# Kernel tuning notes

Hardware: AMD Instinct MI355X
Metric: run time of the kernel (lower is better)

Reference implementation:

```python
import jax, jax.numpy as jnp
import numpy as np

EPS2D = 0.3          # gsplat classic-mode 2D blur added to covariance diagonal
SZ2 = 0.001 ** 2     # sigma_z^2 from the fixed z-scale 0.001
ALPHA_MAX = 0.999    # gsplat alpha clamp


def setup_inputs() -> dict:
    key = jax.random.key(0)
    k0, k1, k2, k3, k4 = jax.random.split(key, 5)
    B, N, H, W = 2, 768, 160, 160
    means = jax.random.uniform(k0, (B, N, 2), jnp.float32, 0.0, float(W))      # pixel coords
    scales = jax.random.uniform(k1, (B, N, 2), jnp.float32, 1.0, 8.0)          # pixel scales
    rotations = jax.random.normal(k2, (B, N, 1), jnp.float32)                  # radians
    colors = jax.random.uniform(k3, (B, N, 3), jnp.float32)                    # RGB [0,1]
    opacities = jax.random.uniform(k4, (B, N, 1), jnp.float32)                 # [0,1]
    return {"means": means, "scales": scales, "rotations": rotations,
            "colors": colors, "opacities": opacities, "H": H, "W": W}


def reference(means, scales, rotations, colors, opacities, H, W):
    B, N, _ = means.shape
    dt = means.dtype
    # quat (cos t/2, 0, 0, sin t/2) == rotation about z by t; cov3d = R diag(sx^2,sy^2,sz^2) R^T
    theta = rotations[..., 0]
    c, s = jnp.cos(theta), jnp.sin(theta)
    sx2, sy2 = scales[..., 0] ** 2, scales[..., 1] ** 2
    a = c * c * sx2 + s * s * sy2            # xy-block of 3D covariance
    b = c * s * (sx2 - sy2)
    d = s * s * sx2 + c * c * sy2
    mx, my = means[..., 0], means[..., 1]
    # viewmat=I, K=I, z=1 -> projected mean = (x, y); Jacobian J = [[1,0,-x],[0,1,-y]]
    # cov2d = J cov3d J^T + eps2d * I  (z-block contributes sz^2 * [x,y] outer [x,y])
    cov_xx = a + SZ2 * mx * mx + EPS2D
    cov_xy = b + SZ2 * mx * my
    cov_yy = d + SZ2 * my * my + EPS2D
    det = cov_xx * cov_yy - cov_xy * cov_xy
    ca, cb, cc = cov_yy / det, -cov_xy / det, cov_xx / det   # conic (inverse cov)

    px = jnp.arange(W, dtype=dt) + 0.5       # pixel centers
    py = jnp.arange(H, dtype=dt) + 0.5
    gx, gy = jnp.meshgrid(px, py)            # (H, W)
    dx = gx.reshape(-1)[None, :, None] - mx[:, None, :]      # (B, HW, N)
    dy = gy.reshape(-1)[None, :, None] - my[:, None, :]
    q = (ca[:, None, :] * dx * dx
         + 2.0 * cb[:, None, :] * dx * dy
         + cc[:, None, :] * dy * dy)
    alpha = jnp.minimum(opacities[:, None, :, 0] * jnp.exp(-0.5 * q), ALPHA_MAX)

    # front-to-back compositing (all depths == 1 -> stable input order)
    log1m = jnp.log1p(-alpha)                                 # (B, HW, N)
    T = jnp.exp(jnp.cumsum(log1m, axis=-1) - log1m)           # exclusive cumprod of (1-alpha)
    w = alpha * T                                             # per-gaussian pixel weight
    img = jnp.einsum('bpn,bnc->bpc', w, colors)               # (B, HW, 3)
    img = img.reshape(B, H, W, 3).transpose(0, 3, 1, 2)       # (B, 3, H, W)
    return jnp.clip(img, 0.0, 1.0)
```

## Files before the change

kernel.cpp:

```cpp
#include <hip/hip_runtime.h>
#include <hip/hip_fp16.h>
#include <string.h>

#define BATCH   2
#define NG      768
#define H_      160
#define W_      160
#define NPIX    (H_ * W_)
#define NCHUNK  8
#define CHUNK   (NG / NCHUNK)
#define TILE    8
#define TPD     (W_ / TILE)
#define NTILE   (TPD * TPD)
#define EPS2D_  0.3f
#define SZ2_    1.0e-6f
#define ALPHA_MAX_ 0.999f
#define KEXP    (-0.7213475204444817f)
#define LN_CULL_EPS (-13.815511f)


__global__ __launch_bounds__(256)
void gr_precompute(const float* __restrict__ means,
                   const float* __restrict__ scales,
                   const float* __restrict__ rots,
                   const float* __restrict__ colors,
                   const float* __restrict__ opac,
                   float4* __restrict__ cull, float4* __restrict__ pay, int total) {
    int i = blockIdx.x * blockDim.x + threadIdx.x;
    if (i >= total) return;
    float theta = rots[i];
    float c = cosf(theta), s = sinf(theta);
    float sx = scales[2*i], sy = scales[2*i+1];
    float sx2 = sx*sx, sy2 = sy*sy;
    float a  = c*c*sx2 + s*s*sy2;
    float bb = c*s*(sx2 - sy2);
    float d  = s*s*sx2 + c*c*sy2;
    float mx = means[2*i], my = means[2*i+1];
    float cxx = a + SZ2_*mx*mx + EPS2D_;
    float cxy = bb + SZ2_*mx*my;
    float cyy = d + SZ2_*my*my + EPS2D_;
    float det = cxx*cyy - cxy*cxy;
    float inv = 1.0f / det;
    float ca  =  cyy * inv;
    float cb2 = -cxy * inv;
    float cc  =  cxx * inv;
    float op  = opac[i];

    float k2 = 2.0f * (logf(op) - LN_CULL_EPS);
    k2 = fmaxf(k2, 0.0f);
    float kk = sqrtf(k2);
    float ex = kk * sqrtf(cxx);
    float ey = kk * sqrtf(cyy);
    cull[i] = make_float4(mx, my, ex, ey);

    float A = KEXP * ca;
    float B = KEXP * 2.0f * cb2;
    float C = KEXP * cc;
    float D = KEXP * (-2.0f * ca * mx - 2.0f * cb2 * my);
    float E = KEXP * (-2.0f * cc * my - 2.0f * cb2 * mx);
    float F = KEXP * (ca*mx*mx + 2.0f*cb2*mx*my + cc*my*my) + log2f(op);
    float cr = colors[3*i], cg = colors[3*i+1], cb = colors[3*i+2];
    __half2 h2 = __floats2half2_rn(cr, cg);
    float rg; memcpy(&rg, &h2, 4);
    pay[2*i]   = make_float4(A, B, C, D);
    pay[2*i+1] = make_float4(E, F, rg, cb);
}

__global__ __launch_bounds__(256)
void gr_render(const float4* __restrict__ cull, const float4* __restrict__ pay,
               float* __restrict__ out) {
    __shared__ float4 stage[4][CHUNK * 2];
    __shared__ float4 partl[4][64];
    int tid  = threadIdx.x;
    int wave = tid >> 6;
    int lane = tid & 63;
    int tile = blockIdx.x;
    int b    = blockIdx.y;
    int tx = tile % TPD, ty = tile / TPD;
    int pxi = tx * TILE + (lane & 7);
    int pyi = ty * TILE + (lane >> 3);
    float px = (float)pxi + 0.5f;
    float py = (float)pyi + 0.5f;
    float cxm = (float)(tx * TILE) + 0.5f * TILE;
    float cym = (float)(ty * TILE) + 0.5f * TILE;
    const float RH = 0.5f * TILE;
    float x2 = px*px, xy = px*py, y2 = py*py;

    float R = 0.f, G = 0.f, B = 0.f, T = 1.f;

    #pragma unroll
    for (int cc = 0; cc < 2; ++cc) {
        int chunk = wave * 2 + cc;
        int base  = b * NG + chunk * CHUNK;
        int cnt = 0;

        {
            float4 cu = cull[base + lane];
            bool keep = (fabsf(cu.x - cxm) <= cu.z + RH) &&
                        (fabsf(cu.y - cym) <= cu.w + RH);
            unsigned long long m = __ballot(keep);
            unsigned pre = __builtin_amdgcn_mbcnt_hi((unsigned)(m >> 32),
                            __builtin_amdgcn_mbcnt_lo((unsigned)m, 0u));
            if (keep) {
                int gi = base + lane;
                stage[wave][2*pre]     = pay[2*gi];
                stage[wave][2*pre + 1] = pay[2*gi + 1];
            }
            cnt = (int)__popcll(m);
        }
        {
            bool valid = lane < (CHUNK - 64);
            int gi = base + 64 + (valid ? lane : 0);
            float4 cu = cull[gi];
            bool keep = valid &&
                        (fabsf(cu.x - cxm) <= cu.z + RH) &&
                        (fabsf(cu.y - cym) <= cu.w + RH);
            unsigned long long m = __ballot(keep);
            unsigned pre = __builtin_amdgcn_mbcnt_hi((unsigned)(m >> 32),
                            __builtin_amdgcn_mbcnt_lo((unsigned)m, 0u));
            if (keep) {
                int slot = cnt + (int)pre;
                stage[wave][2*slot]     = pay[2*gi];
                stage[wave][2*slot + 1] = pay[2*gi + 1];
            }
            cnt += (int)__popcll(m);
        }

        for (int i = 0; i < cnt; ++i) {
            float4 av = stage[wave][2*i];
            float4 ev = stage[wave][2*i + 1];
            float q = fmaf(av.x, x2,
                      fmaf(av.y, xy,
                      fmaf(av.z, y2,
                      fmaf(av.w, px,
                      fmaf(ev.x, py, ev.y)))));
            float al = fminf(__builtin_exp2f(q), ALPHA_MAX_);
            float w  = T * al;
            __half2 h2; memcpy(&h2, &ev.z, 4);
            float2 rg = __half22float2(h2);
            R  = fmaf(w, rg.x, R);
            G  = fmaf(w, rg.y, G);
            B  = fmaf(w, ev.w, B);
            T -= w;
            if (((i & 7) == 7) && __all(T < 1.0e-4f)) break;
        }
        if (__all(T < 1.0e-4f)) break;
    }

    partl[wave][lane] = make_float4(R, G, B, T);
    __syncthreads();

    float4 o = partl[3][lane];
    float r = o.x, g = o.y, bb = o.z;
    #pragma unroll
    for (int i = 2; i >= 0; --i) {
        float4 oi = partl[i][lane];
        r  = fmaf(oi.w, r,  oi.x);
        g  = fmaf(oi.w, g,  oi.y);
        bb = fmaf(oi.w, bb, oi.z);
    }
    if (wave < 3) {
        float v = (wave == 0) ? r : (wave == 1) ? g : bb;
        v = fminf(fmaxf(v, 0.f), 1.f);
        out[(b * 3 + wave) * NPIX + pyi * W_ + pxi] = v;
    }
}

extern "C" void kernel_launch(void* const* d_in, const int* in_sizes, int n_in,
                              void* d_out, int out_size, void* d_ws, size_t ws_size,
                              hipStream_t stream) {
    const float* means  = (const float*)d_in[0];
    const float* scales = (const float*)d_in[1];
    const float* rots   = (const float*)d_in[2];
    const float* colors = (const float*)d_in[3];
    const float* opac   = (const float*)d_in[4];
    float* out = (float*)d_out;

    int total = BATCH * NG;
    float4* cullA = (float4*)d_ws;
    float4* pay   = cullA + total;

    gr_precompute<<<(total + 255) / 256, 256, 0, stream>>>(
        means, scales, rots, colors, opac, cullA, pay, total);

    dim3 rgrid(NTILE, BATCH);
    gr_render<<<rgrid, 256, 0, stream>>>(cullA, pay, out);
}
```

Before: 73.65 us.

## Fuse per-gaussian precompute into render kernel with 8 waves per tile

```diff
diff --git a/kernel.cpp b/kernel.cpp
--- a/kernel.cpp
+++ b/kernel.cpp
@@ -7,8 +7,8 @@
 #define H_      160
 #define W_      160
 #define NPIX    (H_ * W_)
-#define NCHUNK  8
-#define CHUNK   (NG / NCHUNK)
+#define NWAVE   8
+#define CHUNK   (NG / NWAVE)
 #define TILE    8
 #define TPD     (W_ / TILE)
 #define NTILE   (TPD * TPD)
@@ -18,64 +18,61 @@
 #define KEXP    (-0.7213475204444817f)
 #define LN_CULL_EPS (-13.815511f)
 
+__global__ __launch_bounds__(512)
+void gr_fused(const float* __restrict__ means,
+              const float* __restrict__ scales,
+              const float* __restrict__ rots,
+              const float* __restrict__ colors,
+              const float* __restrict__ opac,
+              float* __restrict__ out) {
+    __shared__ float4 ldsCull[NG];
+    __shared__ float4 ldsPay[NG * 2];
+    __shared__ int    ldsIdx[NWAVE][CHUNK];
+    __shared__ float4 partl[NWAVE][64];
 
-__global__ __launch_bounds__(256)
-void gr_precompute(const float* __restrict__ means,
-                   const float* __restrict__ scales,
-                   const float* __restrict__ rots,
-                   const float* __restrict__ colors,
-                   const float* __restrict__ opac,
-                   float4* __restrict__ cull, float4* __restrict__ pay, int total) {
-    int i = blockIdx.x * blockDim.x + threadIdx.x;
-    if (i >= total) return;
-    float theta = rots[i];
-    float c = cosf(theta), s = sinf(theta);
-    float sx = scales[2*i], sy = scales[2*i+1];
-    float sx2 = sx*sx, sy2 = sy*sy;
-    float a  = c*c*sx2 + s*s*sy2;
-    float bb = c*s*(sx2 - sy2);
-    float d  = s*s*sx2 + c*c*sy2;
-    float mx = means[2*i], my = means[2*i+1];
-    float cxx = a + SZ2_*mx*mx + EPS2D_;
-    float cxy = bb + SZ2_*mx*my;
-    float cyy = d + SZ2_*my*my + EPS2D_;
-    float det = cxx*cyy - cxy*cxy;
-    float inv = 1.0f / det;
-    float ca  =  cyy * inv;
-    float cb2 = -cxy * inv;
-    float cc  =  cxx * inv;
-    float op  = opac[i];
-
-    float k2 = 2.0f * (logf(op) - LN_CULL_EPS);
-    k2 = fmaxf(k2, 0.0f);
-    float kk = sqrtf(k2);
-    float ex = kk * sqrtf(cxx);
-    float ey = kk * sqrtf(cyy);
-    cull[i] = make_float4(mx, my, ex, ey);
-
-    float A = KEXP * ca;
-    float B = KEXP * 2.0f * cb2;
-    float C = KEXP * cc;
-    float D = KEXP * (-2.0f * ca * mx - 2.0f * cb2 * my);
-    float E = KEXP * (-2.0f * cc * my - 2.0f * cb2 * mx);
-    float F = KEXP * (ca*mx*mx + 2.0f*cb2*mx*my + cc*my*my) + log2f(op);
-    float cr = colors[3*i], cg = colors[3*i+1], cb = colors[3*i+2];
-    __half2 h2 = __floats2half2_rn(cr, cg);
-    float rg; memcpy(&rg, &h2, 4);
-    pay[2*i]   = make_float4(A, B, C, D);
-    pay[2*i+1] = make_float4(E, F, rg, cb);
-}
-
-__global__ __launch_bounds__(256)
-void gr_render(const float4* __restrict__ cull, const float4* __restrict__ pay,
-               float* __restrict__ out) {
-    __shared__ float4 stage[4][CHUNK * 2];
-    __shared__ float4 partl[4][64];
     int tid  = threadIdx.x;
     int wave = tid >> 6;
     int lane = tid & 63;
     int tile = blockIdx.x;
     int b    = blockIdx.y;
+
+    for (int g = tid; g < NG; g += 512) {
+        int i = b * NG + g;
+        float theta = rots[i];
+        float c = cosf(theta), s = sinf(theta);
+        float sx = scales[2*i], sy = scales[2*i+1];
+        float sx2 = sx*sx, sy2 = sy*sy;
+        float a  = c*c*sx2 + s*s*sy2;
+        float bb = c*s*(sx2 - sy2);
+        float d  = s*s*sx2 + c*c*sy2;
+        float mx = means[2*i], my = means[2*i+1];
+        float cxx = a + SZ2_*mx*mx + EPS2D_;
+        float cxy = bb + SZ2_*mx*my;
+        float cyy = d + SZ2_*my*my + EPS2D_;
+        float det = cxx*cyy - cxy*cxy;
+        float inv = 1.0f / det;
+        float ca  =  cyy * inv;
+        float cb2 = -cxy * inv;
+        float cc  =  cxx * inv;
+        float op  = opac[i];
+
+        float k2 = fmaxf(2.0f * (logf(op) - LN_CULL_EPS), 0.0f);
+        float kk = sqrtf(k2);
+        ldsCull[g] = make_float4(mx, my, kk * sqrtf(cxx), kk * sqrtf(cyy));
+
+        float A = KEXP * ca;
+        float Bq = KEXP * 2.0f * cb2;
+        float C = KEXP * cc;
+        float D = KEXP * (-2.0f * ca * mx - 2.0f * cb2 * my);
+        float E = KEXP * (-2.0f * cc * my - 2.0f * cb2 * mx);
+        float F = KEXP * (ca*mx*mx + 2.0f*cb2*mx*my + cc*my*my) + log2f(op);
+        __half2 h2 = __floats2half2_rn(colors[3*i], colors[3*i+1]);
+        float rg; memcpy(&rg, &h2, 4);
+        ldsPay[2*g]   = make_float4(A, Bq, C, D);
+        ldsPay[2*g+1] = make_float4(E, F, rg, colors[3*i+2]);
+    }
+    __syncthreads();
+
     int tx = tile % TPD, ty = tile / TPD;
     int pxi = tx * TILE + (lane & 7);
     int pyi = ty * TILE + (lane >> 3);
@@ -86,74 +83,59 @@
     const float RH = 0.5f * TILE;
     float x2 = px*px, xy = px*py, y2 = py*py;
 
+    int base = wave * CHUNK;
+    int cnt = 0;
+    {
+        float4 cu = ldsCull[base + lane];
+        bool keep = (fabsf(cu.x - cxm) <= cu.z + RH) &&
+                    (fabsf(cu.y - cym) <= cu.w + RH);
+        unsigned long long m = __ballot(keep);
+        unsigned pre = __builtin_amdgcn_mbcnt_hi((unsigned)(m >> 32),
+                        __builtin_amdgcn_mbcnt_lo((unsigned)m, 0u));
+        if (keep) ldsIdx[wave][pre] = base + lane;
+        cnt = (int)__popcll(m);
+    }
+    {
+        bool valid = lane < (CHUNK - 64);
+        float4 cu = ldsCull[base + 64 + (valid ? lane : 0)];
+        bool keep = valid &&
+                    (fabsf(cu.x - cxm) <= cu.z + RH) &&
+                    (fabsf(cu.y - cym) <= cu.w + RH);
+        unsigned long long m = __ballot(keep);
+        unsigned pre = __builtin_amdgcn_mbcnt_hi((unsigned)(m >> 32),
+                        __builtin_amdgcn_mbcnt_lo((unsigned)m, 0u));
+        if (keep) ldsIdx[wave][cnt + (int)pre] = base + 64 + lane;
+        cnt += (int)__popcll(m);
+    }
+
     float R = 0.f, G = 0.f, B = 0.f, T = 1.f;
-
-    #pragma unroll
-    for (int cc = 0; cc < 2; ++cc) {
-        int chunk = wave * 2 + cc;
-        int base  = b * NG + chunk * CHUNK;
-        int cnt = 0;
-
-        {
-            float4 cu = cull[base + lane];
-            bool keep = (fabsf(cu.x - cxm) <= cu.z + RH) &&
-                        (fabsf(cu.y - cym) <= cu.w + RH);
-            unsigned long long m = __ballot(keep);
-            unsigned pre = __builtin_amdgcn_mbcnt_hi((unsigned)(m >> 32),
-                            __builtin_amdgcn_mbcnt_lo((unsigned)m, 0u));
-            if (keep) {
-                int gi = base + lane;
-                stage[wave][2*pre]     = pay[2*gi];
-                stage[wave][2*pre + 1] = pay[2*gi + 1];
-            }
-            cnt = (int)__popcll(m);
-        }
-        {
-            bool valid = lane < (CHUNK - 64);
-            int gi = base + 64 + (valid ? lane : 0);
-            float4 cu = cull[gi];
-            bool keep = valid &&
-                        (fabsf(cu.x - cxm) <= cu.z + RH) &&
-                        (fabsf(cu.y - cym) <= cu.w + RH);
-            unsigned long long m = __ballot(keep);
-            unsigned pre = __builtin_amdgcn_mbcnt_hi((unsigned)(m >> 32),
-                            __builtin_amdgcn_mbcnt_lo((unsigned)m, 0u));
-            if (keep) {
-                int slot = cnt + (int)pre;
-                stage[wave][2*slot]     = pay[2*gi];
-                stage[wave][2*slot + 1] = pay[2*gi + 1];
-            }
-            cnt += (int)__popcll(m);
-        }
-
-        for (int i = 0; i < cnt; ++i) {
-            float4 av = stage[wave][2*i];
-            float4 ev = stage[wave][2*i + 1];
-            float q = fmaf(av.x, x2,
-                      fmaf(av.y, xy,
-                      fmaf(av.z, y2,
-                      fmaf(av.w, px,
-                      fmaf(ev.x, py, ev.y)))));
-            float al = fminf(__builtin_exp2f(q), ALPHA_MAX_);
-            float w  = T * al;
-            __half2 h2; memcpy(&h2, &ev.z, 4);
-            float2 rg = __half22float2(h2);
-            R  = fmaf(w, rg.x, R);
-            G  = fmaf(w, rg.y, G);
-            B  = fmaf(w, ev.w, B);
-            T -= w;
-            if (((i & 7) == 7) && __all(T < 1.0e-4f)) break;
-        }
-        if (__all(T < 1.0e-4f)) break;
+    for (int i = 0; i < cnt; ++i) {
+        int idx = ldsIdx[wave][i];
+        float4 av = ldsPay[2*idx];
+        float4 ev = ldsPay[2*idx + 1];
+        float q = fmaf(av.x, x2,
+                  fmaf(av.y, xy,
+                  fmaf(av.z, y2,
+                  fmaf(av.w, px,
+                  fmaf(ev.x, py, ev.y)))));
+        float al = fminf(__builtin_exp2f(q), ALPHA_MAX_);
+        float w  = T * al;
+        __half2 h2; memcpy(&h2, &ev.z, 4);
+        float2 rg = __half22float2(h2);
+        R  = fmaf(w, rg.x, R);
+        G  = fmaf(w, rg.y, G);
+        B  = fmaf(w, ev.w, B);
+        T -= w;
+        if (((i & 7) == 7) && __all(T < 1.0e-4f)) break;
     }
 
     partl[wave][lane] = make_float4(R, G, B, T);
     __syncthreads();
 
-    float4 o = partl[3][lane];
+    float4 o = partl[NWAVE-1][lane];
     float r = o.x, g = o.y, bb = o.z;
     #pragma unroll
-    for (int i = 2; i >= 0; --i) {
+    for (int i = NWAVE-2; i >= 0; --i) {
         float4 oi = partl[i][lane];
         r  = fmaf(oi.w, r,  oi.x);
         g  = fmaf(oi.w, g,  oi.y);
@@ -176,13 +158,6 @@
     const float* opac   = (const float*)d_in[4];
     float* out = (float*)d_out;
 
-    int total = BATCH * NG;
-    float4* cullA = (float4*)d_ws;
-    float4* pay   = cullA + total;
-
-    gr_precompute<<<(total + 255) / 256, 256, 0, stream>>>(
-        means, scales, rots, colors, opac, cullA, pay, total);
-
-    dim3 rgrid(NTILE, BATCH);
-    gr_render<<<rgrid, 256, 0, stream>>>(cullA, pay, out);
+    dim3 grid(NTILE, BATCH);
+    gr_fused<<<grid, 512, 0, stream>>>(means, scales, rots, colors, opac, out);
 }
```

Result: no change. 74.37 us (+1.0%).
